# Optimization experiments

Hardware: AMD Instinct MI355X
Metric: run time of the kernel (lower is better)

## Reference

```python
import jax, jax.numpy as jnp
import numpy as np

N_NODES = 100000
C = 128
E = 800000
V = 50000
NEG_SLOPE = 0.2


def gat_conv(x, edges, W, att_src, att_dst, bias, num_nodes):
    """Single-head PyG-style GATConv with self-loops added (PyG default).

    edges: [2, E] with row 0 = source j, row 1 = destination i.
    """
    loops = jnp.arange(num_nodes, dtype=edges.dtype)
    src = jnp.concatenate([edges[0], loops])  # [E+N]
    dst = jnp.concatenate([edges[1], loops])

    h = x @ W.T                               # [N, C] linear transform
    a_s = h @ att_src                         # [N] per-node src score
    a_d = h @ att_dst                         # [N] per-node dst score

    e = jax.nn.leaky_relu(a_s[src] + a_d[dst], NEG_SLOPE)  # [E+N]
    # scatter-softmax over edges grouped by destination node
    m = jax.ops.segment_max(e, dst, num_segments=num_nodes)
    ex = jnp.exp(e - m[dst])
    denom = jax.ops.segment_sum(ex, dst, num_segments=num_nodes)
    alpha = ex / (denom[dst] + 1e-16)         # [E+N]

    out = jax.ops.segment_sum(alpha[:, None] * h[src], dst, num_segments=num_nodes)
    return out + bias


def setup_inputs() -> dict:
    key = jax.random.key(0)
    ks = jax.random.split(key, 12)
    s = 1.0 / np.sqrt(C)
    return {
        "embedding": jax.random.normal(ks[0], (N_NODES, C), jnp.float32),
        "W1": jax.random.normal(ks[1], (C, C), jnp.float32) * s,
        "att_src1": jax.random.normal(ks[2], (C,), jnp.float32) * s,
        "att_dst1": jax.random.normal(ks[3], (C,), jnp.float32) * s,
        "b1": jax.random.normal(ks[4], (C,), jnp.float32) * s,
        "W2": jax.random.normal(ks[5], (C, C), jnp.float32) * s,
        "att_src2": jax.random.normal(ks[6], (C,), jnp.float32) * s,
        "att_dst2": jax.random.normal(ks[7], (C,), jnp.float32) * s,
        "b2": jax.random.normal(ks[8], (C,), jnp.float32) * s,
        "edges1": jax.random.randint(ks[9], (2, E), 0, N_NODES, jnp.int64 if jax.config.jax_enable_x64 else jnp.int32),
        "edges2": jax.random.randint(ks[10], (2, E), 0, N_NODES, jnp.int64 if jax.config.jax_enable_x64 else jnp.int32),
        "idx_mapping": jax.random.randint(ks[11], (V,), 0, N_NODES, jnp.int64 if jax.config.jax_enable_x64 else jnp.int32),
    }


def reference(embedding, W1, att_src1, att_dst1, b1, W2, att_src2, att_dst2, b2,
              edges1, edges2, idx_mapping):
    h = gat_conv(embedding, edges1, W1, att_src1, att_dst1, b1, N_NODES)
    h = gat_conv(h, edges2, W2, att_src2, att_dst2, b2, N_NODES)
    return h[idx_mapping]
```

## Files before the change

kernel.cpp:

```cpp
#include <hip/hip_runtime.h>

#define N_NODES 100000
#define C_DIM 128
#define E_EDGES 800000
#define V_OUT 50000
#define EN (E_EDGES + N_NODES)
#define M2 (2 * N_NODES)
#define EN2 (2 * EN)

#define BSHIFT 9
#define NBUCK_L ((N_NODES + 511) >> 9)
#define NBUCK2 (2 * NBUCK_L)
#define CAP 8192
#define P1_CHUNK 4096
#define P1_PER_T (P1_CHUNK / 256)
#define NCHUNK ((EN2 + P1_CHUNK - 1) / P1_CHUNK)
#define VFLAG_BLKS ((V_OUT + 255) / 256)

#define XPAD 136
#define LDS_E 768

typedef unsigned int uint;
typedef unsigned short ushort;
typedef __attribute__((ext_vector_type(8))) short bf16x8;
typedef __attribute__((ext_vector_type(4))) float f32x4;

static __device__ __forceinline__ ushort f2bf(float f) {
    uint u = __float_as_uint(f);
    u += 0x7fffu + ((u >> 16) & 1);
    return (ushort)(u >> 16);
}

template <int IN_F32>
__global__ __launch_bounds__(256, 4) void gemm_mfma(
    const void* __restrict__ xin, const float* __restrict__ W,
    const float* __restrict__ att_s, const float* __restrict__ att_d,
    ushort* __restrict__ hb, float* __restrict__ a_s, float* __restrict__ a_d)
{
    __shared__ ushort ws[128 * XPAD];
    const int tid = threadIdx.x;

    {
        const int row = tid >> 1, half = tid & 1;
        const float* src = W + row * 128 + half * 64;
        ushort* dst = &ws[row * XPAD + half * 64];
        #pragma unroll
        for (int i = 0; i < 8; ++i) {
            float4 u = *reinterpret_cast<const float4*>(src + i * 8);
            float4 v = *reinterpret_cast<const float4*>(src + i * 8 + 4);
            uint4 pk;
            pk.x = (uint)f2bf(u.x) | ((uint)f2bf(u.y) << 16);
            pk.y = (uint)f2bf(u.z) | ((uint)f2bf(u.w) << 16);
            pk.z = (uint)f2bf(v.x) | ((uint)f2bf(v.y) << 16);
            pk.w = (uint)f2bf(v.z) | ((uint)f2bf(v.w) << 16);
            *reinterpret_cast<uint4*>(dst + i * 8) = pk;
        }
    }

    const int lane = tid & 63, wv = tid >> 6;
    const int m = lane & 15, quad = lane >> 4;
    const int nb = blockIdx.x * 64;
    const int n0 = nb + wv * 16;
    const long xrow = min((long)(n0 + m), (long)N_NODES - 1);

    bf16x8 a[4];
    if (IN_F32) {
        const float* src = (const float*)xin + xrow * 128 + quad * 8;
        #pragma unroll
        for (int ki = 0; ki < 4; ++ki) {
            float4 u = *reinterpret_cast<const float4*>(src + ki * 32);
            float4 v = *reinterpret_cast<const float4*>(src + ki * 32 + 4);
            uint4 pk;
            pk.x = (uint)f2bf(u.x) | ((uint)f2bf(u.y) << 16);
            pk.y = (uint)f2bf(u.z) | ((uint)f2bf(u.w) << 16);
            pk.z = (uint)f2bf(v.x) | ((uint)f2bf(v.y) << 16);
            pk.w = (uint)f2bf(v.z) | ((uint)f2bf(v.w) << 16);
            a[ki] = *reinterpret_cast<bf16x8*>(&pk);
        }
    } else {
        const ushort* src = (const ushort*)xin + xrow * 128 + quad * 8;
        #pragma unroll
        for (int ki = 0; ki < 4; ++ki)
            a[ki] = *reinterpret_cast<const bf16x8*>(src + ki * 32);
    }
    __syncthreads();

    float ps[4] = {0, 0, 0, 0}, pd[4] = {0, 0, 0, 0};
    uint2 packed[8];
    #pragma unroll
    for (int ct = 0; ct < 8; ++ct) {
        const int cc = ct * 16 + m;
        f32x4 acc = {0.f, 0.f, 0.f, 0.f};
        #pragma unroll
        for (int ki = 0; ki < 4; ++ki) {
            bf16x8 b = *reinterpret_cast<const bf16x8*>(&ws[cc * XPAD + quad * 8 + ki * 32]);
            acc = __builtin_amdgcn_mfma_f32_16x16x32_bf16(a[ki], b, acc, 0, 0, 0);
        }
        const float asc = att_s[cc], adc = att_d[cc];
        #pragma unroll
        for (int r = 0; r < 4; ++r) {
            ps[r] = fmaf(acc[r], asc, ps[r]);
            pd[r] = fmaf(acc[r], adc, pd[r]);
        }
        packed[ct].x = (uint)f2bf(acc[0]) | ((uint)f2bf(acc[1]) << 16);
        packed[ct].y = (uint)f2bf(acc[2]) | ((uint)f2bf(acc[3]) << 16);
    }
    __syncthreads();

    {
        const int rowb = (wv * 16 + quad * 4) * XPAD + m;
        #pragma unroll
        for (int ct = 0; ct < 8; ++ct) {
            ws[rowb            + ct * 16] = (ushort)(packed[ct].x);
            ws[rowb +     XPAD + ct * 16] = (ushort)(packed[ct].x >> 16);
            ws[rowb + 2 * XPAD + ct * 16] = (ushort)(packed[ct].y);
            ws[rowb + 3 * XPAD + ct * 16] = (ushort)(packed[ct].y >> 16);
        }
    }
    __syncthreads();

    {
        const int sub = tid & 15, rb = tid >> 4;
        #pragma unroll
        for (int i = 0; i < 4; ++i) {
            const int rl = rb + i * 16;
            const int node = nb + rl;
            uint4 v = *reinterpret_cast<const uint4*>(&ws[rl * XPAD + sub * 8]);
            if (node < N_NODES)
                *reinterpret_cast<uint4*>(hb + (long)node * 128 + sub * 8) = v;
        }
    }
    #pragma unroll
    for (int r = 0; r < 4; ++r) {
        float s = ps[r], d = pd[r];
        #pragma unroll
        for (int x = 1; x < 16; x <<= 1) { s += __shfl_xor(s, x); d += __shfl_xor(d, x); }
        const int node = n0 + quad * 4 + r;
        if (m == 0 && node < N_NODES) { a_s[node] = s; a_d[node] = d; }
    }
}

__global__ __launch_bounds__(256) void partition_kernel(
    const int* __restrict__ e1, const int* __restrict__ e2,
    int* __restrict__ cursor, uint* __restrict__ slab,
    const int* __restrict__ idxm, int* __restrict__ head, int* __restrict__ nextp)
{
    __shared__ int cnt[NBUCK2];
    __shared__ int basearr[NBUCK2];
    const int tid = threadIdx.x;
    const int blk = blockIdx.x;
    if (blk >= NCHUNK) {
        int v = (blk - NCHUNK) * 256 + tid;
        if (v < V_OUT) {
            int n = idxm[v];
            int old = atomicExch(&head[n], v);
            nextp[v] = old;
        }
        return;
    }
    for (int i = tid; i < NBUCK2; i += 256) cnt[i] = 0;
    __syncthreads();

    const int e0 = blk * P1_CHUNK;
    uint ent[P1_PER_T];
    int  bkt[P1_PER_T];
    #pragma unroll
    for (int i = 0; i < P1_PER_T; ++i) {
        int e = e0 + i * 256 + tid;
        bkt[i] = -1;
        if (e < EN2) {
            int src, dst, lb;
            if (e < EN) {
                if (e < E_EDGES) { src = e1[e]; dst = e1[E_EDGES + e]; }
                else             { src = dst = e - E_EDGES; }
                lb = 0;
            } else {
                int f = e - EN;
                if (f < E_EDGES) { src = e2[f]; dst = e2[E_EDGES + f]; }
                else             { src = dst = f - E_EDGES; }
                lb = NBUCK_L;
            }
            bkt[i] = lb + (dst >> BSHIFT);
            ent[i] = (uint)src | ((uint)(dst & 511) << 17);
            atomicAdd(&cnt[bkt[i]], 1);
        }
    }
    __syncthreads();
    for (int b = tid; b < NBUCK2; b += 256) {
        int c = cnt[b];
        basearr[b] = (c > 0) ? atomicAdd(&cursor[b], c) : 0;
        cnt[b] = 0;
    }
    __syncthreads();
    #pragma unroll
    for (int i = 0; i < P1_PER_T; ++i) {
        if (bkt[i] >= 0) {
            int r = basearr[bkt[i]] + atomicAdd(&cnt[bkt[i]], 1);
            if (r < CAP) slab[(long)bkt[i] * CAP + r] = ent[i];
        }
    }
}

__global__ __launch_bounds__(256) void local_csr(
    const uint* __restrict__ slab, const int* __restrict__ cursor,
    int* __restrict__ offs, uint* __restrict__ esrc)
{
    __shared__ uint ent[CAP];
    __shared__ int deg[512];
    __shared__ int excl[512];
    __shared__ int sbase;
    const int b = blockIdx.x;
    const int tid = threadIdx.x;
    const int cnt = min(cursor[b], CAP);
    const int layer = (b >= NBUCK_L);
    const int node0 = (b - layer * NBUCK_L) << BSHIFT;
    const int obase = layer * N_NODES;
    const int nodes_n = min(512, N_NODES - node0);

    for (int i = tid; i < 512; i += 256) deg[i] = 0;
    if (tid < 64) {
        int s = 0;
        #pragma unroll
        for (int k = 0; k < 7; ++k) {
            int idx = tid + 64 * k;
            if (idx < b) s += cursor[idx];
        }
        #pragma unroll
        for (int d = 32; d > 0; d >>= 1) s += __shfl_down(s, d);
        if (tid == 0) sbase = s;
    }
    __syncthreads();
    const int base = sbase;

    for (int i = tid; i < cnt; i += 256) {
        uint v = slab[(long)b * CAP + i];
        ent[i] = v;
        atomicAdd(&deg[v >> 17], 1);
    }
    __syncthreads();
    if (tid < 64) {
        int v8[8]; int s = 0;
        #pragma unroll
        for (int i = 0; i < 8; ++i) { v8[i] = deg[tid * 8 + i]; s += v8[i]; }
        int incl = s;
        #pragma unroll
        for (int d = 1; d < 64; d <<= 1) {
            int t = __shfl_up(incl, d);
            if (tid >= d) incl += t;
        }
        int e = incl - s;
        #pragma unroll
        for (int i = 0; i < 8; ++i) { excl[tid * 8 + i] = e; e += v8[i]; }
    }
    __syncthreads();
    for (int i = tid; i < nodes_n; i += 256)
        offs[obase + node0 + i] = base + excl[i];
    for (int i = tid; i < 512; i += 256) deg[i] = 0;
    if (tid == 0 && node0 + 512 >= N_NODES)
        offs[obase + N_NODES] = base + cnt;
    __syncthreads();
    for (int i = tid; i < cnt; i += 256) {
        uint v = ent[i];
        int dl = v >> 17;
        int r = atomicAdd(&deg[dl], 1);
        esrc[base + excl[dl] + r] = v;
    }
}

template <int MODE>
__global__ __launch_bounds__(256) void aggregate(
    const ushort* __restrict__ hb, const float* __restrict__ a_s,
    const float* __restrict__ a_d, const float* __restrict__ bias,
    const int* __restrict__ offs, const uint* __restrict__ esrc,
    const int* __restrict__ head, const int* __restrict__ nextp,
    void* __restrict__ outp, int obase)
{
    __shared__ uint2 ew[LDS_E];
    const int tid = threadIdx.x;
    const int node0 = blockIdx.x * 16;
    const int bnode0 = (node0 >> BSHIFT) << BSHIFT;
    const int bstart = offs[obase + node0];
    const int bend   = offs[obase + node0 + 16];
    const int nE = bend - bstart;

    for (int i = tid; i < min(nE, LDS_E); i += 256) {
        uint v = esrc[bstart + i];
        float w = 0.0f;
        const int d = bnode0 + (v >> 17);
        if (MODE == 0 || head[d] >= 0) {
            float e = a_s[v & 0x1ffff] + a_d[d];
            e = (e >= 0.0f) ? e : 0.2f * e;
            w = __expf(e);
        }
        ew[i] = make_uint2(v, __float_as_uint(w));
    }
    __syncthreads();

    const int wave = tid >> 6;
    const int lane = tid & 63;
    const int slot = lane >> 4;
    const int c16  = lane & 15;
    const int node = node0 + wave * 4 + slot;
    int hv = 0;
    if (MODE == 1) {
        hv = head[node];
        if (hv < 0) return;
    }

    const int start = offs[obase + node];
    const int end   = offs[obase + node + 1];
    const long coff = (long)(c16 << 3);
    float acc[8] = {0, 0, 0, 0, 0, 0, 0, 0};
    float dsum = 0.0f;

    if (start < end) {
        if (nE <= LDS_E) {
            const int jr = start - bstart, jend = end - bstart;
            const int e1 = jend - 1;
            uint2 p0 = ew[jr];
            uint2 p1 = ew[min(jr + 1, e1)];
            uint2 p2 = ew[min(jr + 2, e1)];
            uint2 p3 = ew[min(jr + 3, e1)];
            uint4 h0 = *reinterpret_cast<const uint4*>(hb + ((long)(p0.x & 0x1ffff) << 7) + coff);
            uint4 h1 = *reinterpret_cast<const uint4*>(hb + ((long)(p1.x & 0x1ffff) << 7) + coff);
            uint4 h2 = *reinterpret_cast<const uint4*>(hb + ((long)(p2.x & 0x1ffff) << 7) + coff);
            uint4 h3 = *reinterpret_cast<const uint4*>(hb + ((long)(p3.x & 0x1ffff) << 7) + coff);
            float w0 = __uint_as_float(p0.y);
            float w1 = __uint_as_float(p1.y);
            float w2 = __uint_as_float(p2.y);
            float w3 = __uint_as_float(p3.y);
            for (int j = jr; j < jend; ++j) {
                uint2 p4 = ew[min(j + 4, e1)];
                uint4 h4 = *reinterpret_cast<const uint4*>(hb + ((long)(p4.x & 0x1ffff) << 7) + coff);
                float w4 = __uint_as_float(p4.y);
                dsum += w0;
                acc[0] = fmaf(w0, __uint_as_float(h0.x << 16),         acc[0]);
                acc[1] = fmaf(w0, __uint_as_float(h0.x & 0xffff0000u), acc[1]);
                acc[2] = fmaf(w0, __uint_as_float(h0.y << 16),         acc[2]);
                acc[3] = fmaf(w0, __uint_as_float(h0.y & 0xffff0000u), acc[3]);
                acc[4] = fmaf(w0, __uint_as_float(h0.z << 16),         acc[4]);
                acc[5] = fmaf(w0, __uint_as_float(h0.z & 0xffff0000u), acc[5]);
                acc[6] = fmaf(w0, __uint_as_float(h0.w << 16),         acc[6]);
                acc[7] = fmaf(w0, __uint_as_float(h0.w & 0xffff0000u), acc[7]);
                w0 = w1; w1 = w2; w2 = w3; w3 = w4;
                h0 = h1; h1 = h2; h2 = h3; h3 = h4;
            }
        } else {
            const float ad = a_d[node];
            for (int j = start; j < end; ++j) {
                uint v = esrc[j];
                float e = a_s[v & 0x1ffff] + ad;
                e = (e >= 0.0f) ? e : 0.2f * e;
                float w = __expf(e);
                uint4 h = *reinterpret_cast<const uint4*>(hb + ((long)(v & 0x1ffff) << 7) + coff);
                dsum += w;
                acc[0] = fmaf(w, __uint_as_float(h.x << 16),         acc[0]);
                acc[1] = fmaf(w, __uint_as_float(h.x & 0xffff0000u), acc[1]);
                acc[2] = fmaf(w, __uint_as_float(h.y << 16),         acc[2]);
                acc[3] = fmaf(w, __uint_as_float(h.y & 0xffff0000u), acc[3]);
                acc[4] = fmaf(w, __uint_as_float(h.z << 16),         acc[4]);
                acc[5] = fmaf(w, __uint_as_float(h.z & 0xffff0000u), acc[5]);
                acc[6] = fmaf(w, __uint_as_float(h.w << 16),         acc[6]);
                acc[7] = fmaf(w, __uint_as_float(h.w & 0xffff0000u), acc[7]);
            }
        }
    }

    const float inv = 1.0f / (dsum + 1e-16f);
    const int c0 = c16 << 3;
    const float4 b0 = *reinterpret_cast<const float4*>(bias + c0);
    const float4 b1 = *reinterpret_cast<const float4*>(bias + c0 + 4);
    float res[8];
    res[0] = fmaf(acc[0], inv, b0.x);
    res[1] = fmaf(acc[1], inv, b0.y);
    res[2] = fmaf(acc[2], inv, b0.z);
    res[3] = fmaf(acc[3], inv, b0.w);
    res[4] = fmaf(acc[4], inv, b1.x);
    res[5] = fmaf(acc[5], inv, b1.y);
    res[6] = fmaf(acc[6], inv, b1.z);
    res[7] = fmaf(acc[7], inv, b1.w);
    if (MODE == 0) {
        uint4 pk;
        pk.x = (uint)f2bf(res[0]) | ((uint)f2bf(res[1]) << 16);
        pk.y = (uint)f2bf(res[2]) | ((uint)f2bf(res[3]) << 16);
        pk.z = (uint)f2bf(res[4]) | ((uint)f2bf(res[5]) << 16);
        pk.w = (uint)f2bf(res[6]) | ((uint)f2bf(res[7]) << 16);
        *reinterpret_cast<uint4*>((ushort*)outp + ((long)node << 7) + c0) = pk;
    } else {
        const float4 r0 = make_float4(res[0], res[1], res[2], res[3]);
        const float4 r1 = make_float4(res[4], res[5], res[6], res[7]);
        for (int v = hv; v >= 0; v = nextp[v]) {
            float* op = (float*)outp + ((long)v << 7) + c0;
            *reinterpret_cast<float4*>(op)     = r0;
            *reinterpret_cast<float4*>(op + 4) = r1;
        }
    }
}

extern "C" void kernel_launch(void* const* d_in, const int* in_sizes, int n_in,
                              void* d_out, int out_size, void* d_ws, size_t ws_size,
                              hipStream_t stream)
{
    const float* emb = (const float*)d_in[0];
    const float* W1  = (const float*)d_in[1];
    const float* as1 = (const float*)d_in[2];
    const float* ad1 = (const float*)d_in[3];
    const float* b1  = (const float*)d_in[4];
    const float* W2  = (const float*)d_in[5];
    const float* as2 = (const float*)d_in[6];
    const float* ad2 = (const float*)d_in[7];
    const float* b2  = (const float*)d_in[8];
    const int* edges1 = (const int*)d_in[9];
    const int* edges2 = (const int*)d_in[10];
    const int* idxm   = (const int*)d_in[11];
    float* out = (float*)d_out;

    char* p = (char*)d_ws;
    auto alloc = [&](size_t bytes) {
        char* r = p;
        p += (bytes + 255) & ~(size_t)255;
        return r;
    };
    ushort* hb   = (ushort*)alloc((size_t)N_NODES * C_DIM * 2);
    ushort* a1o  = (ushort*)alloc((size_t)N_NODES * C_DIM * 2);
    uint*   slab = (uint*)alloc((size_t)NBUCK2 * CAP * 4);
    uint*   esrc = (uint*)alloc((size_t)EN2 * 4);
    int*    offs = (int*)alloc((size_t)(M2 + 1) * 4);
    float*  aS   = (float*)alloc((size_t)N_NODES * 4);
    float*  aD   = (float*)alloc((size_t)N_NODES * 4);
    int*  cursor = (int*)alloc((size_t)NBUCK2 * 4);
    int*  head   = (int*)alloc((size_t)N_NODES * 4);
    int*  nextp  = (int*)alloc((size_t)V_OUT * 4);

    hipMemsetAsync(cursor, 0, (size_t)NBUCK2 * 4, stream);
    hipMemsetAsync(head, 0xFF, (size_t)N_NODES * 4, stream);

    partition_kernel<<<NCHUNK + VFLAG_BLKS, 256, 0, stream>>>(
        edges1, edges2, cursor, slab, idxm, head, nextp);
    local_csr<<<NBUCK2, 256, 0, stream>>>(slab, cursor, offs, esrc);

    gemm_mfma<1><<<(N_NODES + 63) / 64, 256, 0, stream>>>(emb, W1, as1, ad1, hb, aS, aD);
    aggregate<0><<<N_NODES / 16, 256, 0, stream>>>(hb, aS, aD, b1, offs, esrc, head, nextp, a1o, 0);

    gemm_mfma<0><<<(N_NODES + 63) / 64, 256, 0, stream>>>(a1o, W2, as2, ad2, hb, aS, aD);
    aggregate<1><<<N_NODES / 16, 256, 0, stream>>>(hb, aS, aD, b2, offs, esrc, head, nextp, out, N_NODES);
}
```

Baseline: 271.2 us.

## Fuse layer-1 GEMM with edge partitioning and halve CSR bucket size

```diff
diff --git a/kernel.cpp b/kernel.cpp
--- a/kernel.cpp
+++ b/kernel.cpp
@@ -8,10 +8,10 @@
 #define M2 (2 * N_NODES)
 #define EN2 (2 * EN)
 
-#define BSHIFT 9
-#define NBUCK_L ((N_NODES + 511) >> 9)
+#define BSHIFT 8
+#define NBUCK_L ((N_NODES + 255) >> 8)
 #define NBUCK2 (2 * NBUCK_L)
-#define CAP 8192
+#define CAP 4096
 #define P1_CHUNK 4096
 #define P1_PER_T (P1_CHUNK / 256)
 #define NCHUNK ((EN2 + P1_CHUNK - 1) / P1_CHUNK)
@@ -20,6 +20,8 @@
 #define XPAD 136
 #define LDS_E 768
 
+#define GEMM_BLKS ((N_NODES + 63) / 64)
+
 typedef unsigned int uint;
 typedef unsigned short ushort;
 typedef __attribute__((ext_vector_type(8))) short bf16x8;
@@ -32,13 +34,13 @@
 }
 
 template <int IN_F32>
-__global__ __launch_bounds__(256, 4) void gemm_mfma(
+static __device__ __forceinline__ void gemm_body(
+    char* smem, int gb, int tid,
     const void* __restrict__ xin, const float* __restrict__ W,
     const float* __restrict__ att_s, const float* __restrict__ att_d,
     ushort* __restrict__ hb, float* __restrict__ a_s, float* __restrict__ a_d)
 {
-    __shared__ ushort ws[128 * XPAD];
-    const int tid = threadIdx.x;
+    ushort* ws = (ushort*)smem;
 
     {
         const int row = tid >> 1, half = tid & 1;
@@ -59,7 +61,7 @@
 
     const int lane = tid & 63, wv = tid >> 6;
     const int m = lane & 15, quad = lane >> 4;
-    const int nb = blockIdx.x * 64;
+    const int nb = gb * 64;
     const int n0 = nb + wv * 16;
     const long xrow = min((long)(n0 + m), (long)N_NODES - 1);
 
@@ -140,28 +142,17 @@
     }
 }
 
-__global__ __launch_bounds__(256) void partition_kernel(
+static __device__ __forceinline__ void partition_body(
+    char* smem, int pb, int tid,
     const int* __restrict__ e1, const int* __restrict__ e2,
-    int* __restrict__ cursor, uint* __restrict__ slab,
-    const int* __restrict__ idxm, int* __restrict__ head, int* __restrict__ nextp)
-{
-    __shared__ int cnt[NBUCK2];
-    __shared__ int basearr[NBUCK2];
-    const int tid = threadIdx.x;
-    const int blk = blockIdx.x;
-    if (blk >= NCHUNK) {
-        int v = (blk - NCHUNK) * 256 + tid;
-        if (v < V_OUT) {
-            int n = idxm[v];
-            int old = atomicExch(&head[n], v);
-            nextp[v] = old;
-        }
-        return;
-    }
+    int* __restrict__ cursor, uint* __restrict__ slab)
+{
+    int* cnt     = (int*)smem;
+    int* basearr = cnt + NBUCK2;
     for (int i = tid; i < NBUCK2; i += 256) cnt[i] = 0;
     __syncthreads();
 
-    const int e0 = blk * P1_CHUNK;
+    const int e0 = pb * P1_CHUNK;
     uint ent[P1_PER_T];
     int  bkt[P1_PER_T];
     #pragma unroll
@@ -181,7 +172,7 @@
                 lb = NBUCK_L;
             }
             bkt[i] = lb + (dst >> BSHIFT);
-            ent[i] = (uint)src | ((uint)(dst & 511) << 17);
+            ent[i] = (uint)src | ((uint)(dst & 255) << 17);
             atomicAdd(&cnt[bkt[i]], 1);
         }
     }
@@ -201,13 +192,47 @@
     }
 }
 
+__global__ __launch_bounds__(256, 4) void front_kernel(
+    const float* __restrict__ emb, const float* __restrict__ W1,
+    const float* __restrict__ as1, const float* __restrict__ ad1,
+    ushort* __restrict__ hb, float* __restrict__ aS, float* __restrict__ aD,
+    const int* __restrict__ e1, const int* __restrict__ e2,
+    int* __restrict__ cursor, uint* __restrict__ slab,
+    const int* __restrict__ idxm, int* __restrict__ head, int* __restrict__ nextp)
+{
+    __shared__ __attribute__((aligned(16))) char smem[128 * XPAD * 2];
+    const int b = blockIdx.x;
+    const int tid = threadIdx.x;
+    if (b < GEMM_BLKS) {
+        gemm_body<1>(smem, b, tid, emb, W1, as1, ad1, hb, aS, aD);
+    } else if (b < GEMM_BLKS + NCHUNK) {
+        partition_body(smem, b - GEMM_BLKS, tid, e1, e2, cursor, slab);
+    } else {
+        int v = (b - GEMM_BLKS - NCHUNK) * 256 + tid;
+        if (v < V_OUT) {
+            int n = idxm[v];
+            int old = atomicExch(&head[n], v + 1);
+            nextp[v] = old;
+        }
+    }
+}
+
+__global__ __launch_bounds__(256, 4) void gemm2_kernel(
+    const ushort* __restrict__ a1o, const float* __restrict__ W2,
+    const float* __restrict__ as2, const float* __restrict__ ad2,
+    ushort* __restrict__ hb, float* __restrict__ aS, float* __restrict__ aD)
+{
+    __shared__ __attribute__((aligned(16))) char smem[128 * XPAD * 2];
+    gemm_body<0>(smem, blockIdx.x, threadIdx.x, a1o, W2, as2, ad2, hb, aS, aD);
+}
+
 __global__ __launch_bounds__(256) void local_csr(
     const uint* __restrict__ slab, const int* __restrict__ cursor,
     int* __restrict__ offs, uint* __restrict__ esrc)
 {
     __shared__ uint ent[CAP];
-    __shared__ int deg[512];
-    __shared__ int excl[512];
+    __shared__ int deg[256];
+    __shared__ int excl[256];
     __shared__ int sbase;
     const int b = blockIdx.x;
     const int tid = threadIdx.x;
@@ -215,13 +240,13 @@
     const int layer = (b >= NBUCK_L);
     const int node0 = (b - layer * NBUCK_L) << BSHIFT;
     const int obase = layer * N_NODES;
-    const int nodes_n = min(512, N_NODES - node0);
-
-    for (int i = tid; i < 512; i += 256) deg[i] = 0;
+    const int nodes_n = min(256, N_NODES - node0);
+
+    if (tid < 256) deg[tid & 255] = 0;
     if (tid < 64) {
         int s = 0;
         #pragma unroll
-        for (int k = 0; k < 7; ++k) {
+        for (int k = 0; k < 13; ++k) {
             int idx = tid + 64 * k;
             if (idx < b) s += cursor[idx];
         }
@@ -239,9 +264,9 @@
     }
     __syncthreads();
     if (tid < 64) {
-        int v8[8]; int s = 0;
-        #pragma unroll
-        for (int i = 0; i < 8; ++i) { v8[i] = deg[tid * 8 + i]; s += v8[i]; }
+        int v4[4]; int s = 0;
+        #pragma unroll
+        for (int i = 0; i < 4; ++i) { v4[i] = deg[tid * 4 + i]; s += v4[i]; }
         int incl = s;
         #pragma unroll
         for (int d = 1; d < 64; d <<= 1) {
@@ -250,13 +275,13 @@
         }
         int e = incl - s;
         #pragma unroll
-        for (int i = 0; i < 8; ++i) { excl[tid * 8 + i] = e; e += v8[i]; }
+        for (int i = 0; i < 4; ++i) { excl[tid * 4 + i] = e; e += v4[i]; }
     }
     __syncthreads();
     for (int i = tid; i < nodes_n; i += 256)
         offs[obase + node0 + i] = base + excl[i];
-    for (int i = tid; i < 512; i += 256) deg[i] = 0;
-    if (tid == 0 && node0 + 512 >= N_NODES)
+    if (tid < 256) deg[tid & 255] = 0;
+    if (tid == 0 && node0 + 256 >= N_NODES)
         offs[obase + N_NODES] = base + cnt;
     __syncthreads();
     for (int i = tid; i < cnt; i += 256) {
@@ -287,7 +312,7 @@
         uint v = esrc[bstart + i];
         float w = 0.0f;
         const int d = bnode0 + (v >> 17);
-        if (MODE == 0 || head[d] >= 0) {
+        if (MODE == 0 || head[d] != 0) {
             float e = a_s[v & 0x1ffff] + a_d[d];
             e = (e >= 0.0f) ? e : 0.2f * e;
             w = __expf(e);
@@ -304,7 +329,7 @@
     int hv = 0;
     if (MODE == 1) {
         hv = head[node];
-        if (hv < 0) return;
+        if (hv == 0) return;
     }
 
     const int start = offs[obase + node];
@@ -389,8 +414,8 @@
     } else {
         const float4 r0 = make_float4(res[0], res[1], res[2], res[3]);
         const float4 r1 = make_float4(res[4], res[5], res[6], res[7]);
-        for (int v = hv; v >= 0; v = nextp[v]) {
-            float* op = (float*)outp + ((long)v << 7) + c0;
+        for (int v1 = hv; v1 != 0; v1 = nextp[v1 - 1]) {
+            float* op = (float*)outp + ((long)(v1 - 1) << 7) + c0;
             *reinterpret_cast<float4*>(op)     = r0;
             *reinterpret_cast<float4*>(op + 4) = r1;
         }
@@ -428,20 +453,21 @@
     int*    offs = (int*)alloc((size_t)(M2 + 1) * 4);
     float*  aS   = (float*)alloc((size_t)N_NODES * 4);
     float*  aD   = (float*)alloc((size_t)N_NODES * 4);
+    int*  nextp  = (int*)alloc((size_t)V_OUT * 4);
     int*  cursor = (int*)alloc((size_t)NBUCK2 * 4);
     int*  head   = (int*)alloc((size_t)N_NODES * 4);
-    int*  nextp  = (int*)alloc((size_t)V_OUT * 4);
-
-    hipMemsetAsync(cursor, 0, (size_t)NBUCK2 * 4, stream);
-    hipMemsetAsync(head, 0xFF, (size_t)N_NODES * 4, stream);
-
-    partition_kernel<<<NCHUNK + VFLAG_BLKS, 256, 0, stream>>>(
-        edges1, edges2, cursor, slab, idxm, head, nextp);
+
+    hipMemsetAsync(cursor, 0,
+                   (size_t)((char*)head - (char*)cursor) + (size_t)N_NODES * 4, stream);
+
+    front_kernel<<<GEMM_BLKS + NCHUNK + VFLAG_BLKS, 256, 0, stream>>>(
+        emb, W1, as1, ad1, hb, aS, aD, edges1, edges2, cursor, slab,
+        idxm, head, nextp);
+
     local_csr<<<NBUCK2, 256, 0, stream>>>(slab, cursor, offs, esrc);
 
-    gemm_mfma<1><<<(N_NODES + 63) / 64, 256, 0, stream>>>(emb, W1, as1, ad1, hb, aS, aD);
     aggregate<0><<<N_NODES / 16, 256, 0, stream>>>(hb, aS, aD, b1, offs, esrc, head, nextp, a1o, 0);
 
-    gemm_mfma<0><<<(N_NODES + 63) / 64, 256, 0, stream>>>(a1o, W2, as2, ad2, hb, aS, aD);
+    gemm2_kernel<<<GEMM_BLKS, 256, 0, stream>>>(a1o, W2, as2, ad2, hb, aS, aD);
     aggregate<1><<<N_NODES / 16, 256, 0, stream>>>(hb, aS, aD, b2, offs, esrc, head, nextp, out, N_NODES);
 }
```

New measurement: 259.2 us. -4.4%, faster.
